# Kernel tuning notes

Hardware: AMD Instinct MI355X
Metric: run time of the kernel (lower is better)

Reference implementation:

```python
import jax, jax.numpy as jnp
import numpy as np

NUM_CLASSES = 20
K = 5


def setup_inputs() -> dict:
    key = jax.random.key(0)
    k1, k2, k3, k4 = jax.random.split(key, 4)
    x = jax.random.normal(k1, (2, 256, 128, 128), dtype=jnp.float32)
    y = jax.random.uniform(k2, (2, NUM_CLASSES, 128, 128), dtype=jnp.float32)
    memory_x = jax.random.normal(k3, (10000, 256), dtype=jnp.float32)
    memory_y = jax.random.randint(k4, (10000,), 0, NUM_CLASSES, dtype=jnp.int32)
    return {"x": x, "y": y, "memory_x": memory_x, "memory_y": memory_y}


def reference(x, y, memory_x, memory_y):
    # Eval path of kNN.forward: pairwise L2 dist -> top-k smallest -> mode vote -> one-hot.
    b, c, h, w = x.shape
    xf = jnp.transpose(x, (0, 2, 3, 1)).reshape(b * h * w, c)  # [N, c]

    # dist[i,j] = ||xf[i]||^2 + ||mem[j]||^2 - 2 <xf[i], mem[j]>
    x_norm = jnp.sum(xf * xf, axis=1, keepdims=True)            # [N, 1]
    m_norm = jnp.sum(memory_x * memory_x, axis=1)[None, :]      # [1, M]
    dist = x_norm + m_norm - 2.0 * (xf @ memory_x.T)            # [N, M]

    # top-k smallest distances
    _, idx = jax.lax.top_k(-dist, K)                            # [N, K]
    labels = memory_y[idx]                                      # [N, K]

    # mode over the K neighbor labels; ties broken by smallest class id
    # (matches torch.mode, which returns the smallest among most-frequent values)
    counts = jax.nn.one_hot(labels, NUM_CLASSES, dtype=jnp.float32).sum(axis=1)  # [N, C]
    preds = jnp.argmax(counts, axis=1)                          # [N]

    one_hot_preds = jax.nn.one_hot(preds, NUM_CLASSES, dtype=jnp.float32)  # [N, C]
    return jnp.transpose(one_hot_preds.reshape(b, h, w, NUM_CLASSES), (0, 3, 1, 2))
```

## Files before the change

### kernel.cpp

```cpp
#include <hip/hip_runtime.h>
#include <cstdint>

#define NUM_CLASSES 20
#define KSEL 5
#define M_PTS 10000
#define C_DIM 256
#define HW 16384
#define NQB 64
#define NJB 128
#define NT 79
#define MPAD 10112
#define INFV 1e30f

#define WS_MN_OFF 0
#define WS_MW_OFF 40448u
#define WS_XB_OFF 5160448u
#define WS_TOTAL  21937664u

typedef short short8 __attribute__((ext_vector_type(8)));
typedef float f32x4 __attribute__((ext_vector_type(4)));

#define MFMA16(a, b, c) __builtin_amdgcn_mfma_f32_16x16x32_bf16(a, b, c, 0, 0, 0)

__device__ __forceinline__ uint pk2(float a, float b) {
  uint ua = __float_as_uint(a), ub = __float_as_uint(b);
  ua = (ua + 0x7fffu + ((ua >> 16) & 1u)) >> 16;
  ub = (ub + 0x7fffu + ((ub >> 16) & 1u)) >> 16;
  return (ua & 0xffffu) | (ub << 16);
}

__device__ __forceinline__ void gl16(const ushort* g, ushort* l) {
  __builtin_amdgcn_global_load_lds(
      (const __attribute__((address_space(1))) uint*)g,
      (__attribute__((address_space(3))) uint*)l, 16, 0, 0);
}

__global__ void conv_m(const float* __restrict__ mx, ushort* __restrict__ mw,
                       float* __restrict__ mn) {
  const int t = threadIdx.x;
  const int r = blockIdx.x * 64 + (t >> 2);
  const int sg = t & 3;
  if (r >= MPAD) return;
  if (r >= M_PTS) { if (sg == 0) mn[r] = INFV; return; }
  const float4* src = (const float4*)(mx + (size_t)r * C_DIM + sg * 64);
  float4 v[16];
#pragma unroll
  for (int k = 0; k < 16; ++k) v[k] = src[k];
  uint u[32];
  float np = 0.f;
#pragma unroll
  for (int k = 0; k < 16; ++k) {
    u[2 * k]     = pk2(v[k].x, v[k].y);
    u[2 * k + 1] = pk2(v[k].z, v[k].w);
    np = fmaf(v[k].x, v[k].x, np); np = fmaf(v[k].y, v[k].y, np);
    np = fmaf(v[k].z, v[k].z, np); np = fmaf(v[k].w, v[k].w, np);
  }
  uint4* dst = (uint4*)(mw + (size_t)r * C_DIM + sg * 64);
#pragma unroll
  for (int i = 0; i < 8; ++i) dst[i] = *(const uint4*)&u[4 * i];
  np += __shfl_xor(np, 1);
  np += __shfl_xor(np, 2);
  if (sg == 0) mn[r] = np;
}

__global__ void conv_x(const float* __restrict__ x, ushort* __restrict__ xb) {
  const int t = threadIdx.x;
  const int n = blockIdx.x * 64 + (t & 63);
  const int seg = t >> 6;
  const int bb = n >> 14, hw = n & (HW - 1);
  const float* src = x + (size_t)bb * C_DIM * HW + hw;
  uint u[32];
#pragma unroll 8
  for (int k = 0; k < 32; ++k) {
    const int c = seg * 64 + 2 * k;
    const float a0 = src[(size_t)c * HW];
    const float a1 = src[(size_t)(c + 1) * HW];
    u[k] = pk2(a0, a1);
  }
  uint4* dst = (uint4*)(xb + (size_t)n * C_DIM + seg * 64);
#pragma unroll
  for (int i = 0; i < 8; ++i) dst[i] = *(const uint4*)&u[4 * i];
}

__global__ __launch_bounds__(512, 4) void knn_big(
    const float* __restrict__ x, const float* __restrict__ mx,
    const ushort* __restrict__ mw, const float* __restrict__ mn,
    const ushort* __restrict__ xb, const int* __restrict__ my,
    float* __restrict__ out)
{
  __shared__ union {
    ushort As[NJB][C_DIM];
    struct { float Lv[16][KSEL][NQB]; int Lj[16][KSEL][NQB]; } e;
  } sm;

  const int t  = threadIdx.x;
  const int w  = t >> 6;
  const int l  = t & 63;
  const int wj = w >> 1;
  const int wq = w & 1;
  const int lr = l & 15;
  const int lg = l >> 4;

  const int q0  = blockIdx.x * NQB;
  const int bb  = q0 >> 14;
  const int hw0 = q0 & (HW - 1);

  short8 bq[2][8];
#pragma unroll
  for (int qf = 0; qf < 2; ++qf) {
    const ushort* xrow = xb + (size_t)(q0 + wq * 32 + qf * 16 + lr) * C_DIM;
#pragma unroll
    for (int ks = 0; ks < 8; ++ks)
      bq[qf][ks] = *(const short8*)(xrow + ks * 32 + lg * 8);
  }

  float lv[2][KSEL]; int lj[2][KSEL];
#pragma unroll
  for (int qf = 0; qf < 2; ++qf)
#pragma unroll
    for (int e = 0; e < KSEL; ++e) { lv[qf][e] = INFV; lj[qf][e] = 0x7fffffff; }

  const int s_s    = l & 31;
  const int s_rsub = l >> 5;

  const int br0 = wj * 32 + lr;
  const int br1 = br0 + 16;
  const int xr  = lr & 7;

  for (int jt = 0; jt < NT; ++jt) {
    const int j0 = jt * NJB;

    __syncthreads();
#pragma unroll
    for (int i = 0; i < 8; ++i) {
      const int row = w * 16 + 2 * i + s_rsub;
      int jr = j0 + row; if (jr >= M_PTS) jr = M_PTS - 1;
      gl16(mw + (size_t)jr * C_DIM + ((s_s ^ (row & 7)) * 8),
           &sm.As[w * 16 + 2 * i][0]);
    }
    __syncthreads();

    const f32x4 mnr0 = *(const f32x4*)(mn + j0 + wj * 32 + 4 * lg);
    const f32x4 mnr1 = *(const f32x4*)(mn + j0 + wj * 32 + 16 + 4 * lg);

    f32x4 acc[2][2];
#pragma unroll
    for (int jf = 0; jf < 2; ++jf)
#pragma unroll
      for (int qf = 0; qf < 2; ++qf) acc[jf][qf] = (f32x4){0.f, 0.f, 0.f, 0.f};

#pragma unroll
    for (int ks = 0; ks < 8; ++ks) {
      const int k0 = ks * 4 + lg;
      const short8 af0 = *(const short8*)&sm.As[br0][(k0 ^ xr) * 8];
      const short8 af1 = *(const short8*)&sm.As[br1][(k0 ^ xr) * 8];
#pragma unroll
      for (int qf = 0; qf < 2; ++qf) {
        acc[0][qf] = MFMA16(af0, bq[qf][ks], acc[0][qf]);
        acc[1][qf] = MFMA16(af1, bq[qf][ks], acc[1][qf]);
      }
    }

#pragma unroll
    for (int jf = 0; jf < 2; ++jf) {
      const f32x4 mn4 = (jf == 0) ? mnr0 : mnr1;
      const int jb = j0 + wj * 32 + jf * 16 + 4 * lg;
#pragma unroll
      for (int qf = 0; qf < 2; ++qf) {
#pragma unroll
        for (int e = 0; e < 4; ++e) {
          const float sc = fmaf(-2.f, acc[jf][qf][e], mn4[e]);
          if (sc < lv[qf][4]) {
            const int jg = jb + e;
            const float v0 = lv[qf][0], v1 = lv[qf][1], v2 = lv[qf][2], v3 = lv[qf][3];
            const int   i0 = lj[qf][0], i1 = lj[qf][1], i2 = lj[qf][2], i3 = lj[qf][3];
            const bool c0 = sc < v0, c1 = sc < v1, c2 = sc < v2, c3 = sc < v3;
            lv[qf][4] = c3 ? v3 : sc;             lj[qf][4] = c3 ? i3 : jg;
            lv[qf][3] = c3 ? (c2 ? v2 : sc) : v3; lj[qf][3] = c3 ? (c2 ? i2 : jg) : i3;
            lv[qf][2] = c2 ? (c1 ? v1 : sc) : v2; lj[qf][2] = c2 ? (c1 ? i1 : jg) : i2;
            lv[qf][1] = c1 ? (c0 ? v0 : sc) : v1; lj[qf][1] = c1 ? (c0 ? i0 : jg) : i1;
            lv[qf][0] = c0 ? sc : v0;             lj[qf][0] = c0 ? jg : i0;
          }
        }
      }
    }
  }

  __syncthreads();
  {
    const int s = wj * 4 + lg;
#pragma unroll
    for (int qf = 0; qf < 2; ++qf) {
      const int q = wq * 32 + qf * 16 + lr;
#pragma unroll
      for (int e = 0; e < KSEL; ++e) { sm.e.Lv[s][e][q] = lv[qf][e]; sm.e.Lj[s][e][q] = lj[qf][e]; }
    }
  }
  __syncthreads();

  if (t < NQB) {
    float bv[8]; int bj2[8];
#pragma unroll
    for (int k = 0; k < 8; ++k) { bv[k] = INFV; bj2[k] = 0x7fffffff; }
    for (int s = 0; s < 16; ++s) {
#pragma unroll
      for (int e = 0; e < KSEL; ++e) {
        const float v = sm.e.Lv[s][e][t];
        const int  j = sm.e.Lj[s][e][t];
        if (v < bv[7] || (v == bv[7] && j < bj2[7])) {
          int pos = 7;
          while (pos > 0 && (bv[pos - 1] > v || (bv[pos - 1] == v && bj2[pos - 1] > j))) {
            bv[pos] = bv[pos - 1]; bj2[pos] = bj2[pos - 1]; --pos;
          }
          bv[pos] = v; bj2[pos] = j;
        }
      }
    }
    const float *m0 = mx + (size_t)bj2[0] * C_DIM, *m1 = mx + (size_t)bj2[1] * C_DIM;
    const float *m2 = mx + (size_t)bj2[2] * C_DIM, *m3 = mx + (size_t)bj2[3] * C_DIM;
    const float *m4 = mx + (size_t)bj2[4] * C_DIM, *m5 = mx + (size_t)bj2[5] * C_DIM;
    const float *m6 = mx + (size_t)bj2[6] * C_DIM, *m7 = mx + (size_t)bj2[7] * C_DIM;
    const float* xq = x + (size_t)bb * C_DIM * HW + hw0 + t;
    double d0 = 0, d1 = 0, d2 = 0, d3 = 0, d4 = 0, d5 = 0, d6 = 0, d7 = 0;
#pragma unroll 4
    for (int c = 0; c < C_DIM; ++c) {
      const double xv = (double)xq[(size_t)c * HW];
      double dd;
      dd = xv - (double)m0[c]; d0 = fma(dd, dd, d0);
      dd = xv - (double)m1[c]; d1 = fma(dd, dd, d1);
      dd = xv - (double)m2[c]; d2 = fma(dd, dd, d2);
      dd = xv - (double)m3[c]; d3 = fma(dd, dd, d3);
      dd = xv - (double)m4[c]; d4 = fma(dd, dd, d4);
      dd = xv - (double)m5[c]; d5 = fma(dd, dd, d5);
      dd = xv - (double)m6[c]; d6 = fma(dd, dd, d6);
      dd = xv - (double)m7[c]; d7 = fma(dd, dd, d7);
    }
    const double dv[8] = {d0, d1, d2, d3, d4, d5, d6, d7};
    const int    jvv[8] = {bj2[0], bj2[1], bj2[2], bj2[3], bj2[4], bj2[5], bj2[6], bj2[7]};
    int labs[KSEL]; unsigned used = 0;
#pragma unroll
    for (int n = 0; n < KSEL; ++n) {
      double bd = 1e300; int bj = 0x7fffffff; int bk = 0;
#pragma unroll
      for (int k = 0; k < 8; ++k) {
        const bool avail = ((used >> k) & 1u) == 0u;
        if (avail && (dv[k] < bd || (dv[k] == bd && jvv[k] < bj))) {
          bd = dv[k]; bj = jvv[k]; bk = k;
        }
      }
      used |= (1u << bk);
      labs[n] = my[bj];
    }
    int bestLab = NUM_CLASSES, bestCnt = 0;
#pragma unroll
    for (int a = 0; a < KSEL; ++a) {
      int cnt = 0;
#pragma unroll
      for (int b2 = 0; b2 < KSEL; ++b2) cnt += (labs[b2] == labs[a]) ? 1 : 0;
      if (cnt > bestCnt || (cnt == bestCnt && labs[a] < bestLab)) {
        bestCnt = cnt; bestLab = labs[a];
      }
    }
    float* ob = out + (size_t)bb * NUM_CLASSES * HW + hw0 + t;
#pragma unroll
    for (int cls = 0; cls < NUM_CLASSES; ++cls)
      ob[(size_t)cls * HW] = (cls == bestLab) ? 1.0f : 0.0f;
  }
}

#define FNQB 64
#define FNJB 128
#define FNT 79
#define FXP 264
#define FMP 40
__global__ __launch_bounds__(256, 2) void knn_fb(
    const float* __restrict__ x, const float* __restrict__ mx,
    const int* __restrict__ my, float* __restrict__ out)
{
  __shared__ union {
    struct { ushort xs[FNQB][FXP]; ushort ms[FNJB][FMP]; float mnv[FNJB]; } m;
    struct { float Lv[FNQB][8][KSEL]; int Lj[FNQB][8][KSEL]; } e;
  } sm;
  const int t = threadIdx.x, w = t >> 6, l = t & 63;
  const int wj = w >> 1, wq = w & 1, lr = l & 15, lg = l >> 4;
  const int qflat = blockIdx.x * FNQB, bb = qflat >> 14, hw0 = qflat & (HW - 1);
  const float* xbase = x + (size_t)bb * C_DIM * HW + hw0;
  {
    const int q = t & 63, cpb = t >> 6;
#pragma unroll 8
    for (int k = 0; k < 32; ++k) {
      const int cp = cpb + 4 * k;
      ((uint*)&sm.m.xs[q][0])[cp] =
          pk2(xbase[(size_t)(2 * cp) * HW + q], xbase[(size_t)(2 * cp + 1) * HW + q]);
    }
  }
  float lv[2][KSEL]; int lj[2][KSEL]; float thr[2];
#pragma unroll
  for (int qf = 0; qf < 2; ++qf) {
    thr[qf] = INFV;
#pragma unroll
    for (int e = 0; e < KSEL; ++e) { lv[qf][e] = INFV; lj[qf][e] = 0x7fffffff; }
  }
  const int srow = t >> 1, sh = t & 1;
  for (int jt = 0; jt < FNT; ++jt) {
    const int j0 = jt * FNJB;
    f32x4 acc[4][2];
#pragma unroll
    for (int jf = 0; jf < 4; ++jf)
#pragma unroll
      for (int qf = 0; qf < 2; ++qf) acc[jf][qf] = (f32x4){0.f, 0.f, 0.f, 0.f};
    float np = 0.f;
    for (int ks = 0; ks < 8; ++ks) {
      int jr = j0 + srow; jr = (jr < M_PTS) ? jr : (M_PTS - 1);
      const float4* src = (const float4*)(mx + (size_t)jr * C_DIM + ks * 32 + sh * 16);
      const float4 v0 = src[0], v1 = src[1], v2 = src[2], v3 = src[3];
      __syncthreads();
      uint* dst = (uint*)&sm.m.ms[srow][sh * 16];
      dst[0] = pk2(v0.x, v0.y); dst[1] = pk2(v0.z, v0.w);
      dst[2] = pk2(v1.x, v1.y); dst[3] = pk2(v1.z, v1.w);
      dst[4] = pk2(v2.x, v2.y); dst[5] = pk2(v2.z, v2.w);
      dst[6] = pk2(v3.x, v3.y); dst[7] = pk2(v3.z, v3.w);
      np = fmaf(v0.x, v0.x, np); np = fmaf(v0.y, v0.y, np);
      np = fmaf(v0.z, v0.z, np); np = fmaf(v0.w, v0.w, np);
      np = fmaf(v1.x, v1.x, np); np = fmaf(v1.y, v1.y, np);
      np = fmaf(v1.z, v1.z, np); np = fmaf(v1.w, v1.w, np);
      np = fmaf(v2.x, v2.x, np); np = fmaf(v2.y, v2.y, np);
      np = fmaf(v2.z, v2.z, np); np = fmaf(v2.w, v2.w, np);
      np = fmaf(v3.x, v3.x, np); np = fmaf(v3.y, v3.y, np);
      np = fmaf(v3.z, v3.z, np); np = fmaf(v3.w, v3.w, np);
      if (ks == 7) {
        const float full = np + __shfl_xor(np, 1);
        if (sh == 0) sm.m.mnv[srow] = full;
      }
      __syncthreads();
      const short8 bq0 = *(const short8*)&sm.m.xs[wq * 32 + lr][ks * 32 + 8 * lg];
      const short8 bq1 = *(const short8*)&sm.m.xs[wq * 32 + 16 + lr][ks * 32 + 8 * lg];
#pragma unroll
      for (int jf = 0; jf < 4; ++jf) {
        const short8 af = *(const short8*)&sm.m.ms[wj * 64 + jf * 16 + lr][8 * lg];
        acc[jf][0] = MFMA16(af, bq0, acc[jf][0]);
        acc[jf][1] = MFMA16(af, bq1, acc[jf][1]);
      }
    }
#pragma unroll
    for (int jf = 0; jf < 4; ++jf) {
      const f32x4 mn4 = *(const f32x4*)&sm.m.mnv[wj * 64 + jf * 16 + 4 * lg];
      const int jb = j0 + wj * 64 + jf * 16 + 4 * lg;
#pragma unroll
      for (int qf = 0; qf < 2; ++qf) {
#pragma unroll
        for (int e = 0; e < 4; ++e) {
          const int jg = jb + e;
          const float sc = fmaf(-2.f, acc[jf][qf][e], mn4[e]);
          if (jg < M_PTS && sc < thr[qf]) {
            const float v0 = lv[qf][0], v1 = lv[qf][1], v2 = lv[qf][2], v3 = lv[qf][3];
            const int   i0 = lj[qf][0], i1 = lj[qf][1], i2 = lj[qf][2], i3 = lj[qf][3];
            const bool c0 = sc < v0, c1 = sc < v1, c2 = sc < v2, c3 = sc < v3;
            lv[qf][4] = c3 ? v3 : sc;             lj[qf][4] = c3 ? i3 : jg;
            lv[qf][3] = c3 ? (c2 ? v2 : sc) : v3; lj[qf][3] = c3 ? (c2 ? i2 : jg) : i3;
            lv[qf][2] = c2 ? (c1 ? v1 : sc) : v2; lj[qf][2] = c2 ? (c1 ? i1 : jg) : i2;
            lv[qf][1] = c1 ? (c0 ? v0 : sc) : v1; lj[qf][1] = c1 ? (c0 ? i0 : jg) : i1;
            lv[qf][0] = c0 ? sc : v0;             lj[qf][0] = c0 ? jg : i0;
            thr[qf] = lv[qf][4];
          }
        }
      }
    }
  }
  __syncthreads();
#pragma unroll
  for (int qf = 0; qf < 2; ++qf) {
    const int q = wq * 32 + qf * 16 + lr, s = wj * 4 + lg;
#pragma unroll
    for (int e = 0; e < KSEL; ++e) { sm.e.Lv[q][s][e] = lv[qf][e]; sm.e.Lj[q][s][e] = lj[qf][e]; }
  }
  __syncthreads();
  if (t < FNQB) {
    float bv[8]; int bj2[8];
#pragma unroll
    for (int k = 0; k < 8; ++k) { bv[k] = INFV; bj2[k] = 0x7fffffff; }
    for (int s = 0; s < 8; ++s) {
#pragma unroll
      for (int e = 0; e < KSEL; ++e) {
        const float v = sm.e.Lv[t][s][e]; const int j = sm.e.Lj[t][s][e];
        if (v < bv[7] || (v == bv[7] && j < bj2[7])) {
          int pos = 7;
          while (pos > 0 && (bv[pos - 1] > v || (bv[pos - 1] == v && bj2[pos - 1] > j))) {
            bv[pos] = bv[pos - 1]; bj2[pos] = bj2[pos - 1]; --pos;
          }
          bv[pos] = v; bj2[pos] = j;
        }
      }
    }
    const float *m0 = mx + (size_t)bj2[0] * C_DIM, *m1 = mx + (size_t)bj2[1] * C_DIM;
    const float *m2 = mx + (size_t)bj2[2] * C_DIM, *m3 = mx + (size_t)bj2[3] * C_DIM;
    const float *m4 = mx + (size_t)bj2[4] * C_DIM, *m5 = mx + (size_t)bj2[5] * C_DIM;
    const float *m6 = mx + (size_t)bj2[6] * C_DIM, *m7 = mx + (size_t)bj2[7] * C_DIM;
    const float* xq = xbase + t;
    double d0 = 0, d1 = 0, d2 = 0, d3 = 0, d4 = 0, d5 = 0, d6 = 0, d7 = 0;
#pragma unroll 4
    for (int c = 0; c < C_DIM; ++c) {
      const double xv = (double)xq[(size_t)c * HW];
      double dd;
      dd = xv - (double)m0[c]; d0 = fma(dd, dd, d0);
      dd = xv - (double)m1[c]; d1 = fma(dd, dd, d1);
      dd = xv - (double)m2[c]; d2 = fma(dd, dd, d2);
      dd = xv - (double)m3[c]; d3 = fma(dd, dd, d3);
      dd = xv - (double)m4[c]; d4 = fma(dd, dd, d4);
      dd = xv - (double)m5[c]; d5 = fma(dd, dd, d5);
      dd = xv - (double)m6[c]; d6 = fma(dd, dd, d6);
      dd = xv - (double)m7[c]; d7 = fma(dd, dd, d7);
    }
    const double dv[8] = {d0, d1, d2, d3, d4, d5, d6, d7};
    const int jvv[8] = {bj2[0], bj2[1], bj2[2], bj2[3], bj2[4], bj2[5], bj2[6], bj2[7]};
    int labs[KSEL]; unsigned used = 0;
#pragma unroll
    for (int n = 0; n < KSEL; ++n) {
      double bd = 1e300; int bj = 0x7fffffff; int bk = 0;
#pragma unroll
      for (int k = 0; k < 8; ++k) {
        const bool avail = ((used >> k) & 1u) == 0u;
        if (avail && (dv[k] < bd || (dv[k] == bd && jvv[k] < bj))) {
          bd = dv[k]; bj = jvv[k]; bk = k;
        }
      }
      used |= (1u << bk);
      labs[n] = my[bj];
    }
    int bestLab = NUM_CLASSES, bestCnt = 0;
#pragma unroll
    for (int a = 0; a < KSEL; ++a) {
      int cnt = 0;
#pragma unroll
      for (int b2 = 0; b2 < KSEL; ++b2) cnt += (labs[b2] == labs[a]) ? 1 : 0;
      if (cnt > bestCnt || (cnt == bestCnt && labs[a] < bestLab)) { bestCnt = cnt; bestLab = labs[a]; }
    }
    float* ob = out + (size_t)bb * NUM_CLASSES * HW + hw0 + t;
#pragma unroll
    for (int cls = 0; cls < NUM_CLASSES; ++cls)
      ob[(size_t)cls * HW] = (cls == bestLab) ? 1.0f : 0.0f;
  }
}

extern "C" void kernel_launch(void* const* d_in, const int* in_sizes, int n_in,
                              void* d_out, int out_size, void* d_ws, size_t ws_size,
                              hipStream_t stream) {
  (void)in_sizes; (void)n_in; (void)out_size;
  const float* x  = (const float*)d_in[0];
  const float* mx = (const float*)d_in[2];
  const int*   my = (const int*)d_in[3];
  float* out = (float*)d_out;
  if (ws_size >= (size_t)WS_TOTAL) {
    float*  mn = (float*)((char*)d_ws + WS_MN_OFF);
    ushort* mw = (ushort*)((char*)d_ws + WS_MW_OFF);
    ushort* xb = (ushort*)((char*)d_ws + WS_XB_OFF);
    conv_m<<<MPAD / 64, 256, 0, stream>>>(mx, mw, mn);
    conv_x<<<32768 / 64, 256, 0, stream>>>(x, xb);
    knn_big<<<32768 / NQB, 512, 0, stream>>>(x, mx, mw, mn, xb, my, out);
  } else {
    knn_fb<<<32768 / FNQB, 256, 0, stream>>>(x, mx, my, out);
  }
}
```

Measured before the change: 477.0 us.

## Load memory-bank bf16 fragments directly from global instead of staging through LDS

Removes the per-tile LDS staging of the memory-bank tile (global_load_lds plus two block barriers per tile). Each wave now reads its MFMA A-fragments directly from global or L2 with short8 loads and peels the last partial tile to clamp row indices. This drops the block-wide syncs and the LDS traffic, and lowers LDS use, which may help occupancy. In exchange, the two query-group waves sharing each row slice (wq=0,1) now fetch the same rows separately, and global-load latency is exposed inside the MFMA loop with no explicit prefetching.

```diff
diff --git a/kernel.cpp b/kernel.cpp
--- a/kernel.cpp
+++ b/kernel.cpp
@@ -27,12 +27,6 @@
   ua = (ua + 0x7fffu + ((ua >> 16) & 1u)) >> 16;
   ub = (ub + 0x7fffu + ((ub >> 16) & 1u)) >> 16;
   return (ua & 0xffffu) | (ub << 16);
-}
-
-__device__ __forceinline__ void gl16(const ushort* g, ushort* l) {
-  __builtin_amdgcn_global_load_lds(
-      (const __attribute__((address_space(1))) uint*)g,
-      (__attribute__((address_space(3))) uint*)l, 16, 0, 0);
 }
 
 __global__ void conv_m(const float* __restrict__ mx, ushort* __restrict__ mw,
@@ -88,10 +82,7 @@
     const ushort* __restrict__ xb, const int* __restrict__ my,
     float* __restrict__ out)
 {
-  __shared__ union {
-    ushort As[NJB][C_DIM];
-    struct { float Lv[16][KSEL][NQB]; int Lj[16][KSEL][NQB]; } e;
-  } sm;
+  __shared__ struct { float Lv[16][KSEL][NQB]; int Lj[16][KSEL][NQB]; } sm;
 
   const int t  = threadIdx.x;
   const int w  = t >> 6;
@@ -120,28 +111,43 @@
 #pragma unroll
     for (int e = 0; e < KSEL; ++e) { lv[qf][e] = INFV; lj[qf][e] = 0x7fffffff; }
 
-  const int s_s    = l & 31;
-  const int s_rsub = l >> 5;
-
   const int br0 = wj * 32 + lr;
   const int br1 = br0 + 16;
-  const int xr  = lr & 7;
-
-  for (int jt = 0; jt < NT; ++jt) {
-    const int j0 = jt * NJB;
-
-    __syncthreads();
-#pragma unroll
-    for (int i = 0; i < 8; ++i) {
-      const int row = w * 16 + 2 * i + s_rsub;
-      int jr = j0 + row; if (jr >= M_PTS) jr = M_PTS - 1;
-      gl16(mw + (size_t)jr * C_DIM + ((s_s ^ (row & 7)) * 8),
-           &sm.As[w * 16 + 2 * i][0]);
-    }
-    __syncthreads();
-
-    const f32x4 mnr0 = *(const f32x4*)(mn + j0 + wj * 32 + 4 * lg);
-    const f32x4 mnr1 = *(const f32x4*)(mn + j0 + wj * 32 + 16 + 4 * lg);
+
+  const ushort* aw0 = mw + (size_t)br0 * C_DIM + lg * 8;
+  const ushort* aw1 = mw + (size_t)br1 * C_DIM + lg * 8;
+  const float*  mnp = mn + wj * 32 + 4 * lg;
+
+#define SEL_TILE(J0S)                                                         \
+  do {                                                                        \
+    _Pragma("unroll")                                                         \
+    for (int jf = 0; jf < 2; ++jf) {                                          \
+      const f32x4 mn4 = (jf == 0) ? mnr0 : mnr1;                              \
+      const int jb = (J0S) + wj * 32 + jf * 16 + 4 * lg;                      \
+      _Pragma("unroll")                                                       \
+      for (int qf = 0; qf < 2; ++qf) {                                        \
+        _Pragma("unroll")                                                     \
+        for (int e = 0; e < 4; ++e) {                                         \
+          const float sc = fmaf(-2.f, acc[jf][qf][e], mn4[e]);                \
+          if (sc < lv[qf][4]) {    \
+            const int jg = jb + e;                                            \
+            const float v0 = lv[qf][0], v1 = lv[qf][1], v2 = lv[qf][2], v3 = lv[qf][3]; \
+            const int   i0 = lj[qf][0], i1 = lj[qf][1], i2 = lj[qf][2], i3 = lj[qf][3]; \
+            const bool c0 = sc < v0, c1 = sc < v1, c2 = sc < v2, c3 = sc < v3; \
+            lv[qf][4] = c3 ? v3 : sc;             lj[qf][4] = c3 ? i3 : jg;   \
+            lv[qf][3] = c3 ? (c2 ? v2 : sc) : v3; lj[qf][3] = c3 ? (c2 ? i2 : jg) : i3; \
+            lv[qf][2] = c2 ? (c1 ? v1 : sc) : v2; lj[qf][2] = c2 ? (c1 ? i1 : jg) : i2; \
+            lv[qf][1] = c1 ? (c0 ? v0 : sc) : v1; lj[qf][1] = c1 ? (c0 ? i0 : jg) : i1; \
+            lv[qf][0] = c0 ? sc : v0;             lj[qf][0] = c0 ? jg : i0;   \
+          }                                                                   \
+        }                                                                     \
+      }                                                                       \
+    }                                                                         \
+  } while (0)
+
+  for (int jt = 0; jt < NT - 1; ++jt) {
+    const f32x4 mnr0 = *(const f32x4*)(mnp);
+    const f32x4 mnr1 = *(const f32x4*)(mnp + 16);
 
     f32x4 acc[2][2];
 #pragma unroll
@@ -151,9 +157,8 @@
 
 #pragma unroll
     for (int ks = 0; ks < 8; ++ks) {
-      const int k0 = ks * 4 + lg;
-      const short8 af0 = *(const short8*)&sm.As[br0][(k0 ^ xr) * 8];
-      const short8 af1 = *(const short8*)&sm.As[br1][(k0 ^ xr) * 8];
+      const short8 af0 = *(const short8*)(aw0 + ks * 32);
+      const short8 af1 = *(const short8*)(aw1 + ks * 32);
 #pragma unroll
       for (int qf = 0; qf < 2; ++qf) {
         acc[0][qf] = MFMA16(af0, bq[qf][ks], acc[0][qf]);
@@ -161,30 +166,40 @@
       }
     }
 
-#pragma unroll
-    for (int jf = 0; jf < 2; ++jf) {
-      const f32x4 mn4 = (jf == 0) ? mnr0 : mnr1;
-      const int jb = j0 + wj * 32 + jf * 16 + 4 * lg;
+    SEL_TILE(jt * NJB);
+
+    aw0 += NJB * C_DIM; aw1 += NJB * C_DIM; mnp += NJB;
+  }
+
+  {
+    const int j0 = (NT - 1) * NJB;
+    int r0 = j0 + br0; if (r0 >= M_PTS) r0 = M_PTS - 1;
+    int r1 = j0 + br1; if (r1 >= M_PTS) r1 = M_PTS - 1;
+    const ushort* t0 = mw + (size_t)r0 * C_DIM + lg * 8;
+    const ushort* t1 = mw + (size_t)r1 * C_DIM + lg * 8;
+    const f32x4 mnr0 = *(const f32x4*)(mnp);
+    const f32x4 mnr1 = *(const f32x4*)(mnp + 16);
+
+    f32x4 acc[2][2];
+#pragma unroll
+    for (int jf = 0; jf < 2; ++jf)
+#pragma unroll
+      for (int qf = 0; qf < 2; ++qf) acc[jf][qf] = (f32x4){0.f, 0.f, 0.f, 0.f};
+
+#pragma unroll
+    for (int ks = 0; ks < 8; ++ks) {
+      const short8 af0 = *(const short8*)(t0 + ks * 32);
+      const short8 af1 = *(const short8*)(t1 + ks * 32);
 #pragma unroll
       for (int qf = 0; qf < 2; ++qf) {
-#pragma unroll
-        for (int e = 0; e < 4; ++e) {
-          const float sc = fmaf(-2.f, acc[jf][qf][e], mn4[e]);
-          if (sc < lv[qf][4]) {
-            const int jg = jb + e;
-            const float v0 = lv[qf][0], v1 = lv[qf][1], v2 = lv[qf][2], v3 = lv[qf][3];
-            const int   i0 = lj[qf][0], i1 = lj[qf][1], i2 = lj[qf][2], i3 = lj[qf][3];
-            const bool c0 = sc < v0, c1 = sc < v1, c2 = sc < v2, c3 = sc < v3;
-            lv[qf][4] = c3 ? v3 : sc;             lj[qf][4] = c3 ? i3 : jg;
-            lv[qf][3] = c3 ? (c2 ? v2 : sc) : v3; lj[qf][3] = c3 ? (c2 ? i2 : jg) : i3;
-            lv[qf][2] = c2 ? (c1 ? v1 : sc) : v2; lj[qf][2] = c2 ? (c1 ? i1 : jg) : i2;
-            lv[qf][1] = c1 ? (c0 ? v0 : sc) : v1; lj[qf][1] = c1 ? (c0 ? i0 : jg) : i1;
-            lv[qf][0] = c0 ? sc : v0;             lj[qf][0] = c0 ? jg : i0;
-          }
-        }
-      }
-    }
-  }
+        acc[0][qf] = MFMA16(af0, bq[qf][ks], acc[0][qf]);
+        acc[1][qf] = MFMA16(af1, bq[qf][ks], acc[1][qf]);
+      }
+    }
+
+    SEL_TILE(j0);
+  }
+#undef SEL_TILE
 
   __syncthreads();
   {
@@ -193,7 +208,7 @@
     for (int qf = 0; qf < 2; ++qf) {
       const int q = wq * 32 + qf * 16 + lr;
 #pragma unroll
-      for (int e = 0; e < KSEL; ++e) { sm.e.Lv[s][e][q] = lv[qf][e]; sm.e.Lj[s][e][q] = lj[qf][e]; }
+      for (int e = 0; e < KSEL; ++e) { sm.Lv[s][e][q] = lv[qf][e]; sm.Lj[s][e][q] = lj[qf][e]; }
     }
   }
   __syncthreads();
@@ -205,8 +220,8 @@
     for (int s = 0; s < 16; ++s) {
 #pragma unroll
       for (int e = 0; e < KSEL; ++e) {
-        const float v = sm.e.Lv[s][e][t];
-        const int  j = sm.e.Lj[s][e][t];
+        const float v = sm.Lv[s][e][t];
+        const int  j = sm.Lj[s][e][t];
         if (v < bv[7] || (v == bv[7] && j < bj2[7])) {
           int pos = 7;
           while (pos > 0 && (bv[pos - 1] > v || (bv[pos - 1] == v && bj2[pos - 1] > j))) {
```

New measurement: 686.1 us. 1.44x slower.

## Give each wave a private LDS slice and overlap next-tile loads with MFMA

Applied to the files above, without the earlier changes.

The kNN main kernel moves from 512-thread blocks covering 64 queries by 128 memory rows to 256-thread blocks covering 32 queries by 64 rows. Each wave now stages its own 16 memory rows into a private LDS region, which lets it drop the two block-wide __syncthreads per tile and use explicit vmcnt/lgkmcnt waits instead. The next tile's global-to-LDS load is issued after the first half of the K loop has been read into registers, so it overlaps the second half of the MFMAs and the top-k update. In exchange, each memory tile is reused by only 32 queries instead of 64, which doubles global/L2 reads of the memory bank, and the hand-placed waits and scheduling barriers constrain the compiler's scheduling.

```diff
diff --git a/kernel.cpp b/kernel.cpp
--- a/kernel.cpp
+++ b/kernel.cpp
@@ -6,9 +6,9 @@
 #define M_PTS 10000
 #define C_DIM 256
 #define HW 16384
-#define NQB 64
-#define NJB 128
-#define NT 79
+#define NQB 32
+#define NJB 64
+#define NT 158
 #define MPAD 10112
 #define INFV 1e30f
 
@@ -34,6 +34,12 @@
       (const __attribute__((address_space(1))) uint*)g,
       (__attribute__((address_space(3))) uint*)l, 16, 0, 0);
 }
+
+#define VMWAIT0()  do { asm volatile("s_waitcnt vmcnt(0)" ::: "memory"); \
+                        __builtin_amdgcn_sched_barrier(0); } while (0)
+#define LGKM0()    do { asm volatile("s_waitcnt lgkmcnt(0)" ::: "memory"); \
+                        __builtin_amdgcn_sched_barrier(0); } while (0)
+#define SBAR()     __builtin_amdgcn_sched_barrier(0)
 
 __global__ void conv_m(const float* __restrict__ mx, ushort* __restrict__ mw,
                        float* __restrict__ mn) {
@@ -82,22 +88,20 @@
   for (int i = 0; i < 8; ++i) dst[i] = *(const uint4*)&u[4 * i];
 }
 
-__global__ __launch_bounds__(512, 4) void knn_big(
+__global__ __launch_bounds__(256, 4) void knn_big(
     const float* __restrict__ x, const float* __restrict__ mx,
     const ushort* __restrict__ mw, const float* __restrict__ mn,
     const ushort* __restrict__ xb, const int* __restrict__ my,
     float* __restrict__ out)
 {
   __shared__ union {
-    ushort As[NJB][C_DIM];
+    ushort As[4][16][C_DIM];
     struct { float Lv[16][KSEL][NQB]; int Lj[16][KSEL][NQB]; } e;
   } sm;
 
   const int t  = threadIdx.x;
   const int w  = t >> 6;
   const int l  = t & 63;
-  const int wj = w >> 1;
-  const int wq = w & 1;
   const int lr = l & 15;
   const int lg = l >> 4;
 
@@ -108,7 +112,7 @@
   short8 bq[2][8];
 #pragma unroll
   for (int qf = 0; qf < 2; ++qf) {
-    const ushort* xrow = xb + (size_t)(q0 + wq * 32 + qf * 16 + lr) * C_DIM;
+    const ushort* xrow = xb + (size_t)(q0 + qf * 16 + lr) * C_DIM;
 #pragma unroll
     for (int ks = 0; ks < 8; ++ks)
       bq[qf][ks] = *(const short8*)(xrow + ks * 32 + lg * 8);
@@ -122,76 +126,85 @@
 
   const int s_s    = l & 31;
   const int s_rsub = l >> 5;
-
-  const int br0 = wj * 32 + lr;
-  const int br1 = br0 + 16;
-  const int xr  = lr & 7;
+  const int xr     = lr & 7;
+  const float* mnp = mn + w * 16 + 4 * lg;
+  ushort* lds_w = &sm.As[w][0][0];
+
+#define STAGE(J0S) do {                                                       \
+    _Pragma("unroll")                                                         \
+    for (int i_ = 0; i_ < 8; ++i_) {                                          \
+      const int row_ = 2 * i_ + s_rsub;                                       \
+      int jr_ = (J0S) + w * 16 + row_; if (jr_ >= M_PTS) jr_ = M_PTS - 1;     \
+      gl16(mw + (size_t)jr_ * C_DIM + ((s_s ^ (row_ & 7)) * 8),               \
+           lds_w + (2 * i_) * C_DIM);                                         \
+    }                                                                         \
+  } while (0)
+
+  STAGE(0);
 
   for (int jt = 0; jt < NT; ++jt) {
     const int j0 = jt * NJB;
 
-    __syncthreads();
-#pragma unroll
-    for (int i = 0; i < 8; ++i) {
-      const int row = w * 16 + 2 * i + s_rsub;
-      int jr = j0 + row; if (jr >= M_PTS) jr = M_PTS - 1;
-      gl16(mw + (size_t)jr * C_DIM + ((s_s ^ (row & 7)) * 8),
-           &sm.As[w * 16 + 2 * i][0]);
-    }
-    __syncthreads();
-
-    const f32x4 mnr0 = *(const f32x4*)(mn + j0 + wj * 32 + 4 * lg);
-    const f32x4 mnr1 = *(const f32x4*)(mn + j0 + wj * 32 + 16 + 4 * lg);
-
-    f32x4 acc[2][2];
-#pragma unroll
-    for (int jf = 0; jf < 2; ++jf)
-#pragma unroll
-      for (int qf = 0; qf < 2; ++qf) acc[jf][qf] = (f32x4){0.f, 0.f, 0.f, 0.f};
-
-#pragma unroll
-    for (int ks = 0; ks < 8; ++ks) {
-      const int k0 = ks * 4 + lg;
-      const short8 af0 = *(const short8*)&sm.As[br0][(k0 ^ xr) * 8];
-      const short8 af1 = *(const short8*)&sm.As[br1][(k0 ^ xr) * 8];
-#pragma unroll
-      for (int qf = 0; qf < 2; ++qf) {
-        acc[0][qf] = MFMA16(af0, bq[qf][ks], acc[0][qf]);
-        acc[1][qf] = MFMA16(af1, bq[qf][ks], acc[1][qf]);
-      }
-    }
-
-#pragma unroll
-    for (int jf = 0; jf < 2; ++jf) {
-      const f32x4 mn4 = (jf == 0) ? mnr0 : mnr1;
-      const int jb = j0 + wj * 32 + jf * 16 + 4 * lg;
-#pragma unroll
-      for (int qf = 0; qf < 2; ++qf) {
-#pragma unroll
-        for (int e = 0; e < 4; ++e) {
-          const float sc = fmaf(-2.f, acc[jf][qf][e], mn4[e]);
-          if (sc < lv[qf][4]) {
-            const int jg = jb + e;
-            const float v0 = lv[qf][0], v1 = lv[qf][1], v2 = lv[qf][2], v3 = lv[qf][3];
-            const int   i0 = lj[qf][0], i1 = lj[qf][1], i2 = lj[qf][2], i3 = lj[qf][3];
-            const bool c0 = sc < v0, c1 = sc < v1, c2 = sc < v2, c3 = sc < v3;
-            lv[qf][4] = c3 ? v3 : sc;             lj[qf][4] = c3 ? i3 : jg;
-            lv[qf][3] = c3 ? (c2 ? v2 : sc) : v3; lj[qf][3] = c3 ? (c2 ? i2 : jg) : i3;
-            lv[qf][2] = c2 ? (c1 ? v1 : sc) : v2; lj[qf][2] = c2 ? (c1 ? i1 : jg) : i2;
-            lv[qf][1] = c1 ? (c0 ? v0 : sc) : v1; lj[qf][1] = c1 ? (c0 ? i0 : jg) : i1;
-            lv[qf][0] = c0 ? sc : v0;             lj[qf][0] = c0 ? jg : i0;
-          }
-        }
-      }
-    }
-  }
+    VMWAIT0();
+    const f32x4 mn4 = *(const f32x4*)(mnp);
+    mnp += NJB;
+
+    f32x4 acc[2];
+    acc[0] = (f32x4){0.f, 0.f, 0.f, 0.f};
+    acc[1] = (f32x4){0.f, 0.f, 0.f, 0.f};
+
+    short8 fA[4];
+#pragma unroll
+    for (int ks = 0; ks < 4; ++ks)
+      fA[ks] = *(const short8*)(lds_w + lr * C_DIM + ((ks * 4 + lg) ^ xr) * 8);
+#pragma unroll
+    for (int ks = 0; ks < 4; ++ks) {
+      acc[0] = MFMA16(fA[ks], bq[0][ks], acc[0]);
+      acc[1] = MFMA16(fA[ks], bq[1][ks], acc[1]);
+    }
+    short8 fB[4];
+#pragma unroll
+    for (int ks = 0; ks < 4; ++ks)
+      fB[ks] = *(const short8*)(lds_w + lr * C_DIM + (((ks + 4) * 4 + lg) ^ xr) * 8);
+
+    LGKM0();
+    if (jt + 1 < NT) STAGE((jt + 1) * NJB);
+    SBAR();
+
+#pragma unroll
+    for (int ks = 0; ks < 4; ++ks) {
+      acc[0] = MFMA16(fB[ks], bq[0][ks + 4], acc[0]);
+      acc[1] = MFMA16(fB[ks], bq[1][ks + 4], acc[1]);
+    }
+
+    const int jb = j0 + w * 16 + 4 * lg;
+#pragma unroll
+    for (int qf = 0; qf < 2; ++qf) {
+#pragma unroll
+      for (int e = 0; e < 4; ++e) {
+        const float sc = fmaf(-2.f, acc[qf][e], mn4[e]);
+        if (sc < lv[qf][4]) {
+          const int jg = jb + e;
+          const float v0 = lv[qf][0], v1 = lv[qf][1], v2 = lv[qf][2], v3 = lv[qf][3];
+          const int   i0 = lj[qf][0], i1 = lj[qf][1], i2 = lj[qf][2], i3 = lj[qf][3];
+          const bool c0 = sc < v0, c1 = sc < v1, c2 = sc < v2, c3 = sc < v3;
+          lv[qf][4] = c3 ? v3 : sc;             lj[qf][4] = c3 ? i3 : jg;
+          lv[qf][3] = c3 ? (c2 ? v2 : sc) : v3; lj[qf][3] = c3 ? (c2 ? i2 : jg) : i3;
+          lv[qf][2] = c2 ? (c1 ? v1 : sc) : v2; lj[qf][2] = c2 ? (c1 ? i1 : jg) : i2;
+          lv[qf][1] = c1 ? (c0 ? v0 : sc) : v1; lj[qf][1] = c1 ? (c0 ? i0 : jg) : i1;
+          lv[qf][0] = c0 ? sc : v0;             lj[qf][0] = c0 ? jg : i0;
+        }
+      }
+    }
+  }
+#undef STAGE
 
   __syncthreads();
   {
-    const int s = wj * 4 + lg;
+    const int s = w * 4 + lg;
 #pragma unroll
     for (int qf = 0; qf < 2; ++qf) {
-      const int q = wq * 32 + qf * 16 + lr;
+      const int q = qf * 16 + lr;
 #pragma unroll
       for (int e = 0; e < KSEL; ++e) { sm.e.Lv[s][e][q] = lv[qf][e]; sm.e.Lj[s][e][q] = lj[qf][e]; }
     }
@@ -456,7 +469,7 @@
     ushort* xb = (ushort*)((char*)d_ws + WS_XB_OFF);
     conv_m<<<MPAD / 64, 256, 0, stream>>>(mx, mw, mn);
     conv_x<<<32768 / 64, 256, 0, stream>>>(x, xb);
-    knn_big<<<32768 / NQB, 512, 0, stream>>>(x, mx, mw, mn, xb, my, out);
+    knn_big<<<32768 / NQB, 256, 0, stream>>>(x, mx, mw, mn, xb, my, out);
   } else {
     knn_fb<<<32768 / FNQB, 256, 0, stream>>>(x, mx, my, out);
   }
```

Measured after the change: 691.3 us. 1.45x slower.

## Double-buffer memory tiles with async LDS loads and halve the j-tile size

Applied to the files above, without the earlier changes.

Shrinks the memory-point tile from 128 to 64 rows and double-buffers it in LDS, issuing global-to-LDS loads two tiles ahead. Manual vmcnt waits and raw barriers replace the two __syncthreads per iteration, so the next tile's loads can overlap the MFMA and top-k work on the current one. Each wave now computes one 16-row j fragment instead of two, which halves MFMA work per barrier and doubles the number of iterations and barriers. The hand-tuned waitcnt counts depend on the compiler's instruction order, and the next tile is staged before the top-k update, so correctness relies on that ordering.

```diff
diff --git a/kernel.cpp b/kernel.cpp
--- a/kernel.cpp
+++ b/kernel.cpp
@@ -7,8 +7,8 @@
 #define C_DIM 256
 #define HW 16384
 #define NQB 64
-#define NJB 128
-#define NT 79
+#define NJB 64
+#define NT 158
 #define MPAD 10112
 #define INFV 1e30f
 
@@ -34,6 +34,13 @@
       (const __attribute__((address_space(1))) uint*)g,
       (__attribute__((address_space(3))) uint*)l, 16, 0, 0);
 }
+
+#define VMCNT5() do { asm volatile("s_waitcnt vmcnt(5)" ::: "memory"); \
+                      __builtin_amdgcn_sched_barrier(0); } while (0)
+#define VMCNT1() do { asm volatile("s_waitcnt vmcnt(1)" ::: "memory"); \
+                      __builtin_amdgcn_sched_barrier(0); } while (0)
+#define RAWBAR() do { asm volatile("s_barrier" ::: "memory"); \
+                      __builtin_amdgcn_sched_barrier(0); } while (0)
 
 __global__ void conv_m(const float* __restrict__ mx, ushort* __restrict__ mw,
                        float* __restrict__ mn) {
@@ -89,7 +96,7 @@
     float* __restrict__ out)
 {
   __shared__ union {
-    ushort As[NJB][C_DIM];
+    ushort As[2][NJB][C_DIM];
     struct { float Lv[16][KSEL][NQB]; int Lj[16][KSEL][NQB]; } e;
   } sm;
 
@@ -123,68 +130,68 @@
   const int s_s    = l & 31;
   const int s_rsub = l >> 5;
 
-  const int br0 = wj * 32 + lr;
-  const int br1 = br0 + 16;
+  const int br0 = wj * 16 + lr;
   const int xr  = lr & 7;
+
+#define STAGE(J0S, BUF) do {                                                  \
+    _Pragma("unroll")                                                         \
+    for (int i_ = 0; i_ < 4; ++i_) {          \
+      const int row_ = w * 8 + 2 * i_ + s_rsub;                               \
+      int jr_ = (J0S) + row_; if (jr_ >= M_PTS) jr_ = M_PTS - 1;              \
+      gl16(mw + (size_t)jr_ * C_DIM + ((s_s ^ (row_ & 7)) * 8),               \
+           &sm.As[BUF][w * 8 + 2 * i_][0]);                                   \
+    }                                                                         \
+  } while (0)
+
+  STAGE(0, 0);
+  STAGE(NJB, 1);
 
   for (int jt = 0; jt < NT; ++jt) {
     const int j0 = jt * NJB;
-
-    __syncthreads();
-#pragma unroll
-    for (int i = 0; i < 8; ++i) {
-      const int row = w * 16 + 2 * i + s_rsub;
-      int jr = j0 + row; if (jr >= M_PTS) jr = M_PTS - 1;
-      gl16(mw + (size_t)jr * C_DIM + ((s_s ^ (row & 7)) * 8),
-           &sm.As[w * 16 + 2 * i][0]);
-    }
-    __syncthreads();
-
-    const f32x4 mnr0 = *(const f32x4*)(mn + j0 + wj * 32 + 4 * lg);
-    const f32x4 mnr1 = *(const f32x4*)(mn + j0 + wj * 32 + 16 + 4 * lg);
-
-    f32x4 acc[2][2];
-#pragma unroll
-    for (int jf = 0; jf < 2; ++jf)
-#pragma unroll
-      for (int qf = 0; qf < 2; ++qf) acc[jf][qf] = (f32x4){0.f, 0.f, 0.f, 0.f};
+    const int buf = jt & 1;
+
+    const f32x4 mn4 = *(const f32x4*)(mn + j0 + wj * 16 + 4 * lg);
+
+    if (jt < NT - 1) { VMCNT5(); }
+    else            { VMCNT1(); }
+    RAWBAR();
+
+    f32x4 acc[2];
+    acc[0] = (f32x4){0.f, 0.f, 0.f, 0.f};
+    acc[1] = (f32x4){0.f, 0.f, 0.f, 0.f};
 
 #pragma unroll
     for (int ks = 0; ks < 8; ++ks) {
       const int k0 = ks * 4 + lg;
-      const short8 af0 = *(const short8*)&sm.As[br0][(k0 ^ xr) * 8];
-      const short8 af1 = *(const short8*)&sm.As[br1][(k0 ^ xr) * 8];
-#pragma unroll
-      for (int qf = 0; qf < 2; ++qf) {
-        acc[0][qf] = MFMA16(af0, bq[qf][ks], acc[0][qf]);
-        acc[1][qf] = MFMA16(af1, bq[qf][ks], acc[1][qf]);
-      }
-    }
-
-#pragma unroll
-    for (int jf = 0; jf < 2; ++jf) {
-      const f32x4 mn4 = (jf == 0) ? mnr0 : mnr1;
-      const int jb = j0 + wj * 32 + jf * 16 + 4 * lg;
-#pragma unroll
-      for (int qf = 0; qf < 2; ++qf) {
-#pragma unroll
-        for (int e = 0; e < 4; ++e) {
-          const float sc = fmaf(-2.f, acc[jf][qf][e], mn4[e]);
-          if (sc < lv[qf][4]) {
-            const int jg = jb + e;
-            const float v0 = lv[qf][0], v1 = lv[qf][1], v2 = lv[qf][2], v3 = lv[qf][3];
-            const int   i0 = lj[qf][0], i1 = lj[qf][1], i2 = lj[qf][2], i3 = lj[qf][3];
-            const bool c0 = sc < v0, c1 = sc < v1, c2 = sc < v2, c3 = sc < v3;
-            lv[qf][4] = c3 ? v3 : sc;             lj[qf][4] = c3 ? i3 : jg;
-            lv[qf][3] = c3 ? (c2 ? v2 : sc) : v3; lj[qf][3] = c3 ? (c2 ? i2 : jg) : i3;
-            lv[qf][2] = c2 ? (c1 ? v1 : sc) : v2; lj[qf][2] = c2 ? (c1 ? i1 : jg) : i2;
-            lv[qf][1] = c1 ? (c0 ? v0 : sc) : v1; lj[qf][1] = c1 ? (c0 ? i0 : jg) : i1;
-            lv[qf][0] = c0 ? sc : v0;             lj[qf][0] = c0 ? jg : i0;
-          }
-        }
-      }
-    }
-  }
+      const short8 af0 = *(const short8*)&sm.As[buf][br0][(k0 ^ xr) * 8];
+      acc[0] = MFMA16(af0, bq[0][ks], acc[0]);
+      acc[1] = MFMA16(af0, bq[1][ks], acc[1]);
+    }
+
+    RAWBAR();
+    if (jt + 2 < NT) STAGE((jt + 2) * NJB, buf);
+
+    const int jb = j0 + wj * 16 + 4 * lg;
+#pragma unroll
+    for (int qf = 0; qf < 2; ++qf) {
+#pragma unroll
+      for (int e = 0; e < 4; ++e) {
+        const float sc = fmaf(-2.f, acc[qf][e], mn4[e]);
+        if (sc < lv[qf][4]) {
+          const int jg = jb + e;
+          const float v0 = lv[qf][0], v1 = lv[qf][1], v2 = lv[qf][2], v3 = lv[qf][3];
+          const int   i0 = lj[qf][0], i1 = lj[qf][1], i2 = lj[qf][2], i3 = lj[qf][3];
+          const bool c0 = sc < v0, c1 = sc < v1, c2 = sc < v2, c3 = sc < v3;
+          lv[qf][4] = c3 ? v3 : sc;             lj[qf][4] = c3 ? i3 : jg;
+          lv[qf][3] = c3 ? (c2 ? v2 : sc) : v3; lj[qf][3] = c3 ? (c2 ? i2 : jg) : i3;
+          lv[qf][2] = c2 ? (c1 ? v1 : sc) : v2; lj[qf][2] = c2 ? (c1 ? i1 : jg) : i2;
+          lv[qf][1] = c1 ? (c0 ? v0 : sc) : v1; lj[qf][1] = c1 ? (c0 ? i0 : jg) : i1;
+          lv[qf][0] = c0 ? sc : v0;             lj[qf][0] = c0 ? jg : i0;
+        }
+      }
+    }
+  }
+#undef STAGE
 
   __syncthreads();
   {
```

Result: faster. 449.6 us (median of 3 runs) (-5.8%).
